# Optimization experiments

Hardware: AMD Instinct MI355X
Metric: run time of the kernel (lower is better)

The kernel has to match this reference:

```python
import jax, jax.numpy as jnp
import numpy as np

BETA_MAX = 5.0


def setup_inputs() -> dict:
    key = jax.random.key(0)
    ks = jax.random.split(key, 10)
    N, M, R, d, NTAU, G = 100000, 1000000, 4, 16, 16, 128
    return {
        "c_3": jax.random.randint(ks[0], (M,), 0, N),
        "u_3": jax.random.randint(ks[1], (M,), 0, N),
        "v_3": jax.random.randint(ks[2], (M,), 0, N),
        "t_tau": jax.random.randint(ks[3], (M,), 0, NTAU),
        "batch": jnp.sort(jax.random.randint(ks[4], (N,), 0, G)),
        "Q3": jax.random.normal(ks[5], (N, R, d), dtype=jnp.float32),
        "K3": jax.random.normal(ks[6], (N, R, d), dtype=jnp.float32),
        "T_params": jax.random.normal(ks[7], (NTAU, d), dtype=jnp.float32),
        "raw_lambda_3": jax.random.uniform(ks[8], (1,), dtype=jnp.float32),
        "raw_beta_3": jax.random.uniform(ks[9], (1,), dtype=jnp.float32),
        "num_nodes": N,
        "num_graphs": G,
    }


def reference(c_3, u_3, v_3, t_tau, batch, Q3, K3, T_params,
              raw_lambda_3, raw_beta_3, num_nodes, num_graphs):
    R, d = Q3.shape[-2], Q3.shape[-1]
    scale = (R * d) ** 0.5
    lam = jax.nn.softplus(raw_lambda_3[0])            # positive_param
    beta = jnp.minimum(jax.nn.softplus(raw_beta_3[0]), BETA_MAX)  # inverse_temperature

    # fused motif dot: gather Q/K by triangle indices, contract over d -> [M, R]
    T_sel = T_params[t_tau]                           # [M, d]
    ell = jnp.einsum('mrd,mrd,mrd,md->mr', Q3[c_3], K3[u_3], K3[v_3], T_sel) / scale
    z = beta * ell                                    # [M, R]

    # segment logsumexp over center-node segments c_3 -> [num_nodes, R]
    seg_max = jax.ops.segment_max(z, c_3, num_segments=num_nodes)
    safe_max = jnp.where(jnp.isfinite(seg_max), seg_max, 0.0)
    sums = jax.ops.segment_sum(jnp.exp(z - safe_max[c_3]), c_3, num_segments=num_nodes)
    lse = jnp.where(sums > 0, safe_max + jnp.log(jnp.where(sums > 0, sums, 1.0)), 0.0)

    # scatter-add node lse into graphs -> [num_graphs, R]
    graph_lse = jax.ops.segment_sum(lse, batch, num_segments=num_graphs)
    return (lam / beta) * graph_lse
```

## Files before the change

### kernel.cpp

```cpp
#include <hip/hip_runtime.h>
#include <hip/hip_fp16.h>


#define RR 4
#define DD 16
#define BETA_MAX 5.0f

typedef float v2f __attribute__((ext_vector_type(2)));

__device__ __forceinline__ float softplus_f(float x) {
    return log1pf(__expf(x));
}

__device__ __forceinline__ int pack4_fp8(float4 f) {
    int w = 0;
    w = __builtin_amdgcn_cvt_pk_fp8_f32(f.x, f.y, w, false);
    w = __builtin_amdgcn_cvt_pk_fp8_f32(f.z, f.w, w, true);
    return w;
}

__global__ void me_init_convert(const float* __restrict__ raw_lam,
                                const float* __restrict__ raw_beta,
                                const float* __restrict__ Q3,
                                const float* __restrict__ K3,
                                int4* __restrict__ Q8, int4* __restrict__ K8,
                                float* __restrict__ scal, float* __restrict__ sums,
                                float* __restrict__ out,
                                int n16each, int nr, int out_size) {
    int i = blockIdx.x * blockDim.x + threadIdx.x;
    if (i == 0) {
        float beta = fminf(softplus_f(raw_beta[0]), BETA_MAX);
        float lam  = softplus_f(raw_lam[0]);
        scal[0] = beta * 0.125f;
        scal[1] = lam / beta;
    }
    if (i < nr) sums[i] = 0.0f;
    if (i < out_size) out[i] = 0.0f;
    if (i < 2 * n16each) {
        const float* src = (i < n16each) ? Q3 : K3;
        int4*        dst = (i < n16each) ? Q8 : K8;
        int j = (i < n16each) ? i : i - n16each;
        const float4* s4 = (const float4*)src + 4 * (size_t)j;
        int4 o;
        o.x = pack4_fp8(s4[0]);
        o.y = pack4_fp8(s4[1]);
        o.z = pack4_fp8(s4[2]);
        o.w = pack4_fp8(s4[3]);
        dst[j] = o;
    }
}

__device__ __forceinline__ float dot16_fp8(int4 q8, int4 u8, int4 v8,
                                           const float* __restrict__ Trow) {
    float acc = 0.0f;
    const int qw[4] = {q8.x, q8.y, q8.z, q8.w};
    const int uw[4] = {u8.x, u8.y, u8.z, u8.w};
    const int vw[4] = {v8.x, v8.y, v8.z, v8.w};
#pragma unroll
    for (int j = 0; j < 4; ++j) {
        v2f ql = __builtin_amdgcn_cvt_pk_f32_fp8(qw[j], false);
        v2f qh = __builtin_amdgcn_cvt_pk_f32_fp8(qw[j], true);
        v2f ul = __builtin_amdgcn_cvt_pk_f32_fp8(uw[j], false);
        v2f uh = __builtin_amdgcn_cvt_pk_f32_fp8(uw[j], true);
        v2f vl = __builtin_amdgcn_cvt_pk_f32_fp8(vw[j], false);
        v2f vh = __builtin_amdgcn_cvt_pk_f32_fp8(vw[j], true);
        const float4 tw = *(const float4*)(Trow + 4 * j);
        acc += ql.x * ul.x * vl.x * tw.x + ql.y * ul.y * vl.y * tw.y +
               qh.x * uh.x * vh.x * tw.z + qh.y * uh.y * vh.y * tw.w;
    }
    return acc;
}

__global__ void me_motif_8(const int* __restrict__ c3, const int* __restrict__ u3,
                           const int* __restrict__ v3, const int* __restrict__ tt,
                           const int4* __restrict__ Q8, const int4* __restrict__ K8,
                           const float* __restrict__ Tp, const float* __restrict__ scal,
                           float* __restrict__ sums, int M) {
    int tid = blockIdx.x * blockDim.x + threadIdx.x;
    int m = tid >> 2;
    if (m >= M) return;
    int k = tid & 3;

    int c = c3[m], u = u3[m], v = v3[m], t = tt[m];
    float bscale = scal[0];

    int4 q8 = Q8[(size_t)c * 4 + k];
    int4 u8 = K8[(size_t)u * 4 + k];
    int4 v8 = K8[(size_t)v * 4 + k];

    float p = dot16_fp8(q8, u8, v8, Tp + (size_t)t * DD);
    atomicAdd(&sums[c * RR + k], __expf(bscale * p));
}

__global__ void me_motif_f32(const int* __restrict__ c3, const int* __restrict__ u3,
                             const int* __restrict__ v3, const int* __restrict__ tt,
                             const float* __restrict__ Q3, const float* __restrict__ K3,
                             const float* __restrict__ Tp, const float* __restrict__ scal,
                             float* __restrict__ sums, int M) {
    int tid = blockIdx.x * blockDim.x + threadIdx.x;
    int m = tid >> 4;
    if (m >= M) return;
    int l = tid & 15;
    int r = l >> 2;
    int off = r * DD + ((l & 3) << 2);
    int dc  = (l & 3) << 2;

    int c = c3[m], u = u3[m], v = v3[m], t = tt[m];
    float bscale = scal[0];

    const float4 q  = *(const float4*)(Q3 + ((size_t)c * (RR * DD) + off));
    const float4 ku = *(const float4*)(K3 + ((size_t)u * (RR * DD) + off));
    const float4 kv = *(const float4*)(K3 + ((size_t)v * (RR * DD) + off));
    const float4 tw = *(const float4*)(Tp + ((size_t)t * DD + dc));

    float p = q.x * ku.x * kv.x * tw.x + q.y * ku.y * kv.y * tw.y +
              q.z * ku.z * kv.z * tw.z + q.w * ku.w * kv.w * tw.w;
    p += __shfl_xor(p, 1);
    p += __shfl_xor(p, 2);

    if ((l & 3) == 0) atomicAdd(&sums[c * RR + r], __expf(bscale * p));
}

__global__ void me_init_f32(const float* __restrict__ raw_lam,
                            const float* __restrict__ raw_beta,
                            float* __restrict__ scal, float* __restrict__ sums,
                            float* __restrict__ out, int nr, int out_size) {
    int i = blockIdx.x * blockDim.x + threadIdx.x;
    if (i == 0) {
        float beta = fminf(softplus_f(raw_beta[0]), BETA_MAX);
        float lam  = softplus_f(raw_lam[0]);
        scal[0] = beta * 0.125f;
        scal[1] = lam / beta;
    }
    if (i < nr) sums[i] = 0.0f;
    if (i < out_size) out[i] = 0.0f;
}

__global__ void me_node(const float* __restrict__ sums, const int* __restrict__ batch,
                        const float* __restrict__ scal, float* __restrict__ out,
                        int N, int out_size) {
    extern __shared__ float acc[];
    for (int i = threadIdx.x; i < out_size; i += blockDim.x) acc[i] = 0.0f;
    __syncthreads();

    int total = N * RR;
    for (int tid = blockIdx.x * blockDim.x + threadIdx.x; tid < total;
         tid += gridDim.x * blockDim.x) {
        int n = tid >> 2, r = tid & 3;
        float s = sums[tid];
        if (s > 0.0f) atomicAdd(&acc[batch[n] * RR + r], logf(s));
    }
    __syncthreads();

    float coef = scal[1];
    for (int i = threadIdx.x; i < out_size; i += blockDim.x) {
        float a = acc[i];
        if (a != 0.0f) atomicAdd(&out[i], a * coef);
    }
}

extern "C" void kernel_launch(void* const* d_in, const int* in_sizes, int n_in,
                              void* d_out, int out_size, void* d_ws, size_t ws_size,
                              hipStream_t stream) {
    const int*   c3    = (const int*)d_in[0];
    const int*   u3    = (const int*)d_in[1];
    const int*   v3    = (const int*)d_in[2];
    const int*   tt    = (const int*)d_in[3];
    const int*   batch = (const int*)d_in[4];
    const float* Q3    = (const float*)d_in[5];
    const float* K3    = (const float*)d_in[6];
    const float* Tp    = (const float*)d_in[7];
    const float* rlam  = (const float*)d_in[8];
    const float* rbeta = (const float*)d_in[9];

    const int M   = in_sizes[0];
    const int nel = in_sizes[5];
    const int N   = nel / (RR * DD);
    const int nr  = N * RR;

    const size_t fp8_bytes = (size_t)nel;
    const size_t need = 2 * fp8_bytes + (2 + (size_t)nr) * sizeof(float);

    float* out = (float*)d_out;

    if (ws_size >= need) {
        int4*  Q8   = (int4*)d_ws;
        int4*  K8   = (int4*)((char*)d_ws + fp8_bytes);
        float* scal = (float*)((char*)d_ws + 2 * fp8_bytes);
        float* sums = scal + 2;

        const int n16each = nel / 16;
        {
            int tot = 2 * n16each;
            if (nr > tot) tot = nr;
            me_init_convert<<<(tot + 255) / 256, 256, 0, stream>>>(
                rlam, rbeta, Q3, K3, Q8, K8, scal, sums, out, n16each, nr, out_size);
        }
        {
            long long threads = (long long)M * 4;
            int blocks = (int)((threads + 255) / 256);
            me_motif_8<<<blocks, 256, 0, stream>>>(c3, u3, v3, tt, Q8, K8, Tp, scal, sums, M);
        }
        me_node<<<256, 256, (size_t)out_size * sizeof(float), stream>>>(
            sums, batch, scal, out, N, out_size);
    } else {
        float* scal = (float*)d_ws;
        float* sums = scal + 2;
        {
            int tot = nr > out_size ? nr : out_size;
            me_init_f32<<<(tot + 255) / 256, 256, 0, stream>>>(rlam, rbeta, scal, sums, out, nr, out_size);
        }
        {
            long long threads = (long long)M * 16;
            int blocks = (int)((threads + 255) / 256);
            me_motif_f32<<<blocks, 256, 0, stream>>>(c3, u3, v3, tt, Q3, K3, Tp, scal, sums, M);
        }
        me_node<<<256, 256, (size_t)out_size * sizeof(float), stream>>>(
            sums, batch, scal, out, N, out_size);
    }
}
```

Measured before the change: 186.8 us.

## Process two motifs per thread, use nontemporal index loads, vectorize node and convert kernels

The motif kernel now handles two motif entries per thread (m and m+half), with nontemporal loads for the index streams. This gives more memory-level parallelism for the random fp8 gathers and avoids polluting the cache with streaming data. The convert kernel switches to one float4 per thread with nontemporal loads. The node kernel reads a float4 of sums per node, so batch is loaded once per node instead of once per element. Scalars are padded to 4 floats so sums is 16-byte aligned for the vector load.

```diff
diff --git a/kernel.cpp b/kernel.cpp
--- a/kernel.cpp
+++ b/kernel.cpp
@@ -1,5 +1,4 @@
 #include <hip/hip_runtime.h>
-#include <hip/hip_fp16.h>
 
 
 #define RR 4
@@ -7,12 +6,23 @@
 #define BETA_MAX 5.0f
 
 typedef float v2f __attribute__((ext_vector_type(2)));
+typedef float v4f __attribute__((ext_vector_type(4)));
+
+#if defined(__has_builtin)
+#if __has_builtin(__builtin_nontemporal_load)
+#define NT_LOAD(p) __builtin_nontemporal_load(p)
+#else
+#define NT_LOAD(p) (*(p))
+#endif
+#else
+#define NT_LOAD(p) (*(p))
+#endif
 
 __device__ __forceinline__ float softplus_f(float x) {
     return log1pf(__expf(x));
 }
 
-__device__ __forceinline__ int pack4_fp8(float4 f) {
+__device__ __forceinline__ int pack4_fp8(v4f f) {
     int w = 0;
     w = __builtin_amdgcn_cvt_pk_fp8_f32(f.x, f.y, w, false);
     w = __builtin_amdgcn_cvt_pk_fp8_f32(f.z, f.w, w, true);
@@ -23,10 +33,10 @@
                                 const float* __restrict__ raw_beta,
                                 const float* __restrict__ Q3,
                                 const float* __restrict__ K3,
-                                int4* __restrict__ Q8, int4* __restrict__ K8,
+                                int* __restrict__ Q8, int* __restrict__ K8,
                                 float* __restrict__ scal, float* __restrict__ sums,
                                 float* __restrict__ out,
-                                int n16each, int nr, int out_size) {
+                                int n4each, int nr, int out_size) {
     int i = blockIdx.x * blockDim.x + threadIdx.x;
     if (i == 0) {
         float beta = fminf(softplus_f(raw_beta[0]), BETA_MAX);
@@ -36,17 +46,12 @@
     }
     if (i < nr) sums[i] = 0.0f;
     if (i < out_size) out[i] = 0.0f;
-    if (i < 2 * n16each) {
-        const float* src = (i < n16each) ? Q3 : K3;
-        int4*        dst = (i < n16each) ? Q8 : K8;
-        int j = (i < n16each) ? i : i - n16each;
-        const float4* s4 = (const float4*)src + 4 * (size_t)j;
-        int4 o;
-        o.x = pack4_fp8(s4[0]);
-        o.y = pack4_fp8(s4[1]);
-        o.z = pack4_fp8(s4[2]);
-        o.w = pack4_fp8(s4[3]);
-        dst[j] = o;
+    if (i < 2 * n4each) {
+        const float* src = (i < n4each) ? Q3 : K3;
+        int*         dst = (i < n4each) ? Q8 : K8;
+        int j = (i < n4each) ? i : i - n4each;
+        v4f f = NT_LOAD((const v4f*)src + j);
+        dst[j] = pack4_fp8(f);
     }
 }
 
@@ -64,32 +69,50 @@
         v2f uh = __builtin_amdgcn_cvt_pk_f32_fp8(uw[j], true);
         v2f vl = __builtin_amdgcn_cvt_pk_f32_fp8(vw[j], false);
         v2f vh = __builtin_amdgcn_cvt_pk_f32_fp8(vw[j], true);
-        const float4 tw = *(const float4*)(Trow + 4 * j);
+        const v4f tw = *(const v4f*)(Trow + 4 * j);
         acc += ql.x * ul.x * vl.x * tw.x + ql.y * ul.y * vl.y * tw.y +
                qh.x * uh.x * vh.x * tw.z + qh.y * uh.y * vh.y * tw.w;
     }
     return acc;
 }
 
-__global__ void me_motif_8(const int* __restrict__ c3, const int* __restrict__ u3,
-                           const int* __restrict__ v3, const int* __restrict__ tt,
-                           const int4* __restrict__ Q8, const int4* __restrict__ K8,
-                           const float* __restrict__ Tp, const float* __restrict__ scal,
-                           float* __restrict__ sums, int M) {
+__global__ __launch_bounds__(256)
+void me_motif_8(const int* __restrict__ c3, const int* __restrict__ u3,
+                const int* __restrict__ v3, const int* __restrict__ tt,
+                const int4* __restrict__ Q8, const int4* __restrict__ K8,
+                const float* __restrict__ Tp, const float* __restrict__ scal,
+                float* __restrict__ sums, int M, int half) {
     int tid = blockIdx.x * blockDim.x + threadIdx.x;
-    int m = tid >> 2;
-    if (m >= M) return;
+    int m0 = tid >> 2;
+    if (m0 >= half) return;
     int k = tid & 3;
-
-    int c = c3[m], u = u3[m], v = v3[m], t = tt[m];
+    int m1 = m0 + half;
+    bool has1 = (m1 < M);
+    int m1c = has1 ? m1 : m0;
+
+    int c0 = NT_LOAD(c3 + m0);
+    int u0 = NT_LOAD(u3 + m0);
+    int v0 = NT_LOAD(v3 + m0);
+    int t0 = NT_LOAD(tt + m0);
+    int c1 = NT_LOAD(c3 + m1c);
+    int u1 = NT_LOAD(u3 + m1c);
+    int v1 = NT_LOAD(v3 + m1c);
+    int t1 = NT_LOAD(tt + m1c);
+
     float bscale = scal[0];
 
-    int4 q8 = Q8[(size_t)c * 4 + k];
-    int4 u8 = K8[(size_t)u * 4 + k];
-    int4 v8 = K8[(size_t)v * 4 + k];
-
-    float p = dot16_fp8(q8, u8, v8, Tp + (size_t)t * DD);
-    atomicAdd(&sums[c * RR + k], __expf(bscale * p));
+    int4 q0 = Q8[(size_t)c0 * 4 + k];
+    int4 a0 = K8[(size_t)u0 * 4 + k];
+    int4 b0 = K8[(size_t)v0 * 4 + k];
+    int4 q1 = Q8[(size_t)c1 * 4 + k];
+    int4 a1 = K8[(size_t)u1 * 4 + k];
+    int4 b1 = K8[(size_t)v1 * 4 + k];
+
+    float p0 = dot16_fp8(q0, a0, b0, Tp + (size_t)t0 * DD);
+    float p1 = dot16_fp8(q1, a1, b1, Tp + (size_t)t1 * DD);
+
+    atomicAdd(&sums[c0 * RR + k], __expf(bscale * p0));
+    if (has1) atomicAdd(&sums[c1 * RR + k], __expf(bscale * p1));
 }
 
 __global__ void me_motif_f32(const int* __restrict__ c3, const int* __restrict__ u3,
@@ -143,12 +166,14 @@
     for (int i = threadIdx.x; i < out_size; i += blockDim.x) acc[i] = 0.0f;
     __syncthreads();
 
-    int total = N * RR;
-    for (int tid = blockIdx.x * blockDim.x + threadIdx.x; tid < total;
-         tid += gridDim.x * blockDim.x) {
-        int n = tid >> 2, r = tid & 3;
-        float s = sums[tid];
-        if (s > 0.0f) atomicAdd(&acc[batch[n] * RR + r], logf(s));
+    for (int n = blockIdx.x * blockDim.x + threadIdx.x; n < N;
+         n += gridDim.x * blockDim.x) {
+        v4f s = *((const v4f*)sums + n);
+        int g = batch[n] * RR;
+        if (s.x > 0.0f) atomicAdd(&acc[g + 0], logf(s.x));
+        if (s.y > 0.0f) atomicAdd(&acc[g + 1], logf(s.y));
+        if (s.z > 0.0f) atomicAdd(&acc[g + 2], logf(s.z));
+        if (s.w > 0.0f) atomicAdd(&acc[g + 3], logf(s.w));
     }
     __syncthreads();
 
@@ -179,33 +204,41 @@
     const int nr  = N * RR;
 
     const size_t fp8_bytes = (size_t)nel;
-    const size_t need = 2 * fp8_bytes + (2 + (size_t)nr) * sizeof(float);
+    const size_t need = 2 * fp8_bytes + (4 + (size_t)nr) * sizeof(float);
 
     float* out = (float*)d_out;
 
     if (ws_size >= need) {
-        int4*  Q8   = (int4*)d_ws;
-        int4*  K8   = (int4*)((char*)d_ws + fp8_bytes);
+        int*   Q8   = (int*)d_ws;
+        int*   K8   = (int*)((char*)d_ws + fp8_bytes);
         float* scal = (float*)((char*)d_ws + 2 * fp8_bytes);
-        float* sums = scal + 2;
-
-        const int n16each = nel / 16;
-        {
-            int tot = 2 * n16each;
+        float* sums = scal + 4;
+
+        const int n4each = nel / 4;
+        {
+            int tot = 2 * n4each;
             if (nr > tot) tot = nr;
+            if (out_size > tot) tot = out_size;
             me_init_convert<<<(tot + 255) / 256, 256, 0, stream>>>(
-                rlam, rbeta, Q3, K3, Q8, K8, scal, sums, out, n16each, nr, out_size);
-        }
-        {
-            long long threads = (long long)M * 4;
+                rlam, rbeta, Q3, K3, Q8, K8, scal, sums, out, n4each, nr, out_size);
+        }
+        {
+            const int half = (M + 1) / 2;
+            long long threads = (long long)half * 4;
             int blocks = (int)((threads + 255) / 256);
-            me_motif_8<<<blocks, 256, 0, stream>>>(c3, u3, v3, tt, Q8, K8, Tp, scal, sums, M);
-        }
-        me_node<<<256, 256, (size_t)out_size * sizeof(float), stream>>>(
-            sums, batch, scal, out, N, out_size);
+            me_motif_8<<<blocks, 256, 0, stream>>>(c3, u3, v3, tt, (const int4*)Q8,
+                                                   (const int4*)K8, Tp, scal, sums,
+                                                   M, half);
+        }
+        {
+            int nblk = (N + 255) / 256;
+            if (nblk > 256) nblk = 256;
+            me_node<<<nblk, 256, (size_t)out_size * sizeof(float), stream>>>(
+                sums, batch, scal, out, N, out_size);
+        }
     } else {
         float* scal = (float*)d_ws;
-        float* sums = scal + 2;
+        float* sums = scal + 4;
         {
             int tot = nr > out_size ? nr : out_size;
             me_init_f32<<<(tot + 255) / 256, 256, 0, stream>>>(rlam, rbeta, scal, sums, out, nr, out_size);
@@ -215,7 +248,11 @@
             int blocks = (int)((threads + 255) / 256);
             me_motif_f32<<<blocks, 256, 0, stream>>>(c3, u3, v3, tt, Q3, K3, Tp, scal, sums, M);
         }
-        me_node<<<256, 256, (size_t)out_size * sizeof(float), stream>>>(
-            sums, batch, scal, out, N, out_size);
-    }
-}
+        {
+            int nblk = (N + 255) / 256;
+            if (nblk > 256) nblk = 256;
+            me_node<<<nblk, 256, (size_t)out_size * sizeof(float), stream>>>(
+                sums, batch, scal, out, N, out_size);
+        }
+    }
+}
```

Result: faster. 180.6 us (median of 2 runs) (-3.3%).
